# Optimization experiments

Measured on AMD Instinct MI355X. Metric: run time of the kernel, lower is better.

## Reference

```python
import jax, jax.numpy as jnp
import numpy as np
import math

D, H = 128, 8
B, LC, LQ = 8, 512, 64


def pos_signal(channels, length):
    # tensor2tensor timing signal, returned as [C, L]
    pos = jnp.arange(length, dtype=jnp.float32)
    nts = channels // 2
    inc = math.log(1.0e4) / (nts - 1)
    inv = jnp.exp(jnp.arange(nts, dtype=jnp.float32) * -inc)
    st = pos[:, None] * inv[None, :]                      # [L, nts]
    sig = jnp.concatenate([jnp.sin(st), jnp.cos(st)], 1)  # [L, C]
    return sig.T


def mask_logits(t, m):
    return t * m + (1.0 - m) * -1e30


def ln_c(x, g, b):  # LayerNorm over channel dim of [B, D, L]
    mu = jnp.mean(x, axis=1, keepdims=True)
    var = jnp.mean((x - mu) ** 2, axis=1, keepdims=True)
    return (x - mu) / jnp.sqrt(var + 1e-5) * g[None, :, None] + b[None, :, None]


def conv1x1(x, w, b=None):  # x [B, I, L], w [O, I]
    y = jnp.einsum('oi,bil->bol', w, x)
    return y if b is None else y + b[None, :, None]


def dw_sep_conv(x, dw, pw, pwb):  # depthwise (k, no bias) -> pointwise (bias) -> relu
    k = dw.shape[-1]
    y = jax.lax.conv_general_dilated(x, dw[:, None, :], (1,), [(k // 2, k // 2)],
        dimension_numbers=('NCH', 'OIH', 'NCH'), feature_group_count=x.shape[1])
    return jax.nn.relu(conv1x1(y, pw, pwb))


def self_attention(x, mem_w, q_w, mask, n_head):  # x [B, D, L]
    b, d, L = x.shape
    dh = d // n_head
    mem = jnp.einsum('oi,bil->blo', mem_w, x)  # [B, L, 2D]
    q = jnp.einsum('oi,bil->blo', q_w, x)      # [B, L, D]
    def heads(t):
        return t.reshape(b, L, n_head, dh).transpose(0, 2, 1, 3)  # [B, H, L, dh]
    Qh = heads(q) * dh ** -0.5
    K = heads(mem[..., :d])
    V = heads(mem[..., d:])
    logits = jnp.einsum('bhqe,bhke->bhqk', Qh, K)
    logits = mask_logits(logits, mask[:, None, None, :])
    w = jax.nn.softmax(logits, axis=-1)
    o = jnp.einsum('bhqk,bhke->bhqe', w, V)
    return o.transpose(0, 2, 1, 3).reshape(b, L, d).transpose(0, 2, 1)


def encoder_block(x, mask, p, n_head):
    out = x + pos_signal(x.shape[1], x.shape[2])[None]
    n_conv = p['dw'].shape[0]
    for i in range(n_conv):
        res = out
        out = ln_c(out, p['lnc_g'][i], p['lnc_b'][i])
        out = dw_sep_conv(out, p['dw'][i], p['pw'][i], p['pw_b'][i]) + res
    res = out
    out = ln_c(out, p['ln1_g'], p['ln1_b'])
    out = self_attention(out, p['mem_w'], p['q_w'], mask, n_head) + res
    res = out
    out = ln_c(out, p['ln2_g'], p['ln2_b'])
    out = jax.nn.relu(conv1x1(out, p['ffn1_w'], p['ffn1_b']))
    out = conv1x1(out, p['ffn2_w'], p['ffn2_b'])
    return out + res


def cq_attention(Ce, Qe, cmask, qmask, w4C, w4Q, w4mlu, cq_b):
    Cx = Ce.transpose(0, 2, 1)   # [B, Lc, 2D]
    Qx = Qe.transpose(0, 2, 1)   # [B, Lq, 2D]
    s0 = jnp.einsum('bld,d->bl', Cx, w4C)[:, :, None]
    s1 = jnp.einsum('bqd,d->bq', Qx, w4Q)[:, None, :]
    s2 = jnp.einsum('bld,bqd->blq', Cx * w4mlu[None, None, :], Qx)
    S = s0 + s1 + s2 + cq_b
    S1 = jax.nn.softmax(mask_logits(S, qmask[:, None, :]), axis=2)
    S2 = jax.nn.softmax(mask_logits(S, cmask[:, :, None]), axis=1)
    A = jnp.einsum('blq,bqd->bld', S1, Qx)
    Bt = jnp.einsum('blq,bmq,bmd->bld', S1, S2, Cx)  # (S1 @ S2^T) @ C
    out = jnp.concatenate([Cx, A, Cx * A, Cx * Bt], axis=2)
    return out.transpose(0, 2, 1)  # [B, 8D, Lc]


def _forward(C, Q, maskC, maskQ, e_dw, e_pw, e_pw_b, e_lnc_g, e_lnc_b, e_mem_w, e_q_w,
             e_ffn1_w, e_ffn1_b, e_ffn2_w, e_ffn2_b, e_ln1_g, e_ln1_b, e_ln2_g, e_ln2_b,
             w4C, w4Q, w4mlu, cq_b, resizer_w,
             m_dw, m_pw, m_pw_b, m_lnc_g, m_lnc_b, m_mem_w, m_q_w,
             m_ffn1_w, m_ffn1_b, m_ffn2_w, m_ffn2_b, m_ln1_g, m_ln1_b, m_ln2_g, m_ln2_b):
    ep = dict(dw=e_dw, pw=e_pw, pw_b=e_pw_b, lnc_g=e_lnc_g, lnc_b=e_lnc_b,
              mem_w=e_mem_w, q_w=e_q_w, ffn1_w=e_ffn1_w, ffn1_b=e_ffn1_b,
              ffn2_w=e_ffn2_w, ffn2_b=e_ffn2_b, ln1_g=e_ln1_g, ln1_b=e_ln1_b,
              ln2_g=e_ln2_g, ln2_b=e_ln2_b)
    mp = dict(dw=m_dw, pw=m_pw, pw_b=m_pw_b, lnc_g=m_lnc_g, lnc_b=m_lnc_b,
              mem_w=m_mem_w, q_w=m_q_w, ffn1_w=m_ffn1_w, ffn1_b=m_ffn1_b,
              ffn2_w=m_ffn2_w, ffn2_b=m_ffn2_b, ln1_g=m_ln1_g, ln1_b=m_ln1_b,
              ln2_g=m_ln2_g, ln2_b=m_ln2_b)
    Ce = encoder_block(C, maskC, ep, H)
    Qe = encoder_block(Q, maskQ, ep, H)
    Ce = jnp.concatenate([Ce, C], axis=1)  # encode_fusion -> [B, 2D, Lc]
    Qe = jnp.concatenate([Qe, Q], axis=1)
    X = cq_attention(Ce, Qe, maskC, maskQ, w4C, w4Q, w4mlu, cq_b)
    X = jnp.concatenate([X, Ce], axis=1)   # match_fusion -> [B, 10D, Lc]
    M0 = conv1x1(X, resizer_w)             # [B, D, Lc]

    def run(m):
        def step(carry, p):
            return encoder_block(carry, maskC, p, H), None
        m, _ = jax.lax.scan(step, m, mp)
        return m

    M1 = run(M0)
    M2 = run(M1)
    M3 = run(M2)
    return M1, M2, M3


def setup_inputs() -> dict:
    key = jax.random.key(0)
    ks = iter(jax.random.split(key, 48))
    def rn(shape, scale):
        return jax.random.normal(next(ks), shape, dtype=jnp.float32) * scale
    s1 = 1.0 / math.sqrt(D)
    s2 = 1.0 / math.sqrt(2 * D)
    f32 = jnp.float32
    return dict(
        C=rn((B, D, LC), 1.0), Q=rn((B, D, LQ), 1.0),
        maskC=jnp.ones((B, LC), f32), maskQ=jnp.ones((B, LQ), f32),
        e_dw=rn((4, D, 7), 1.0 / math.sqrt(7)), e_pw=rn((4, D, D), s1),
        e_pw_b=jnp.zeros((4, D), f32), e_lnc_g=jnp.ones((4, D), f32), e_lnc_b=jnp.zeros((4, D), f32),
        e_mem_w=rn((2 * D, D), s1), e_q_w=rn((D, D), s1),
        e_ffn1_w=rn((D, D), s1), e_ffn1_b=jnp.zeros((D,), f32),
        e_ffn2_w=rn((D, D), s1), e_ffn2_b=jnp.zeros((D,), f32),
        e_ln1_g=jnp.ones((D,), f32), e_ln1_b=jnp.zeros((D,), f32),
        e_ln2_g=jnp.ones((D,), f32), e_ln2_b=jnp.zeros((D,), f32),
        w4C=rn((2 * D,), s2), w4Q=rn((2 * D,), s2), w4mlu=rn((2 * D,), s2),
        cq_b=jnp.zeros((1,), f32),
        resizer_w=rn((D, 10 * D), 1.0 / math.sqrt(10 * D)),
        m_dw=rn((7, 2, D, 5), 1.0 / math.sqrt(5)), m_pw=rn((7, 2, D, D), s1),
        m_pw_b=jnp.zeros((7, 2, D), f32), m_lnc_g=jnp.ones((7, 2, D), f32), m_lnc_b=jnp.zeros((7, 2, D), f32),
        m_mem_w=rn((7, 2 * D, D), s1), m_q_w=rn((7, D, D), s1),
        m_ffn1_w=rn((7, D, D), s1), m_ffn1_b=jnp.zeros((7, D), f32),
        m_ffn2_w=rn((7, D, D), s1), m_ffn2_b=jnp.zeros((7, D), f32),
        m_ln1_g=jnp.ones((7, D), f32), m_ln1_b=jnp.zeros((7, D), f32),
        m_ln2_g=jnp.ones((7, D), f32), m_ln2_b=jnp.zeros((7, D), f32),
    )


def reference(C, Q, maskC, maskQ, e_dw, e_pw, e_pw_b, e_lnc_g, e_lnc_b, e_mem_w, e_q_w,
              e_ffn1_w, e_ffn1_b, e_ffn2_w, e_ffn2_b, e_ln1_g, e_ln1_b, e_ln2_g, e_ln2_b,
              w4C, w4Q, w4mlu, cq_b, resizer_w,
              m_dw, m_pw, m_pw_b, m_lnc_g, m_lnc_b, m_mem_w, m_q_w,
              m_ffn1_w, m_ffn1_b, m_ffn2_w, m_ffn2_b, m_ln1_g, m_ln1_b, m_ln2_g, m_ln2_b):
    return _forward(C, Q, maskC, maskQ, e_dw, e_pw, e_pw_b, e_lnc_g, e_lnc_b, e_mem_w, e_q_w,
                    e_ffn1_w, e_ffn1_b, e_ffn2_w, e_ffn2_b, e_ln1_g, e_ln1_b, e_ln2_g, e_ln2_b,
                    w4C, w4Q, w4mlu, cq_b, resizer_w,
                    m_dw, m_pw, m_pw_b, m_lnc_g, m_lnc_b, m_mem_w, m_q_w,
                    m_ffn1_w, m_ffn1_b, m_ffn2_w, m_ffn2_b, m_ln1_g, m_ln1_b, m_ln2_g, m_ln2_b)
```

## Files before the change

### kernel.cpp

```cpp
#include <hip/hip_runtime.h>
#include <math.h>

#define D_  128
#define B_  8
#define H_  8
#define LC_ 512
#define LQ_ 64

typedef float f32x4 __attribute__((ext_vector_type(4)));
typedef short bf16x8 __attribute__((ext_vector_type(8)));
typedef short short4v __attribute__((ext_vector_type(4)));
typedef unsigned short ushortT;

__device__ inline short bfr(float x) {
  unsigned u = __float_as_uint(x);
  u += 0x7fff + ((u >> 16) & 1);
  return (short)(u >> 16);
}
__device__ inline float bfi(ushortT u) {
  return __uint_as_float(((unsigned)u) << 16);
}

__device__ inline bf16x8 mk8(short4v lo, short4v hi) {
  bf16x8 r;
// ... 6 lines not shown
  short4v lo = *(const short4v*)(row + koff);
  short4v hi = *(const short4v*)(row + koff + 16);
  return mk8(lo, hi);
}
__device__ inline bf16x8 ldB2(const ushortT* plo, const ushortT* phi) {
  short4v lo = *(const short4v*)plo;
  short4v hi = *(const short4v*)phi;
  return mk8(lo, hi);
}

__global__ void k_prep(const float* a0, const float* a1, const float* a2,
                       const float* a3, const float* a4, const float* a5,
                       const float* a6, const float* a7, const float* a8,
                       const float* a9, const float* a10, ushortT* dst) {
  int i = blockIdx.x * 256 + threadIdx.x;
  if (i >= 1114112) return;
  const float* s; int lo;
  if      (i <   65536) { s = a0;  lo = i; }
  else if (i <   98304) { s = a1;  lo = i - 65536; }
  else if (i <  114688) { s = a2;  lo = i - 98304; }
  else if (i <  131072) { s = a3;  lo = i - 114688; }
  else if (i <  147456) { s = a4;  lo = i - 131072; }
  else if (i <  311296) { s = a5;  lo = i - 147456; }
  else if (i <  540672) { s = a6;  lo = i - 311296; }
  else if (i <  770048) { s = a7;  lo = i - 540672; }
  else if (i <  884736) { s = a8;  lo = i - 770048; }
  else if (i <  999424) { s = a9;  lo = i - 884736; }
  else                  { s = a10; lo = i - 999424; }
  dst[i] = (ushortT)bfr(s[lo]);
}

template <int KK, int ADDPOS>
__global__ __launch_bounds__(256) void k_fusedconv(
    const float* __restrict__ x, float* __restrict__ yout,
    const float* __restrict__ dw1, const ushortT* __restrict__ pw1,
    const float* __restrict__ pb1, const float* __restrict__ g1,
    const float* __restrict__ be1,
    const float* __restrict__ dw2, const ushortT* __restrict__ pw2,
    const float* __restrict__ pb2, const float* __restrict__ g2w,
    const float* __restrict__ be2, int L) {
  const int HALO = KK / 2;
  const int W1 = 32 + 2 * HALO;
  __shared__ __align__(16) float raw[128 * 40];
  __shared__ __align__(16) ushortT l1o[128 * 36];
  __shared__ __align__(16) ushortT xbf1[32 * 32 * 4];
  __shared__ float mu1[40], rs1[40], mu2[32], rs2[32], ps[160], psq[160];
  ushortT* xbf2 = (ushortT*)raw;
  int l0 = blockIdx.x * 16;
  int o0 = blockIdx.y * 64;
  int b = blockIdx.z;
  int tid = threadIdx.x;
  for (int idx = tid; idx < 128 * W1; idx += 256) {
    int d = idx / W1, c = idx - d * W1;
    int gl = l0 - 8 - HALO + c;
    float v = 0.f;
    if (gl >= 0 && gl < L) {
      v = x[((size_t)b * 128 + d) * L + gl];
      if (ADDPOS) {
        int j = d & 63;
        float arg = (float)gl * expf(-(float)j * 0.14619588f);
        v += (d < 64) ? sinf(arg) : cosf(arg);
      }
    }
    raw[d * 40 + c] = v;
  }
  __syncthreads();
  if (tid < 4 * W1) {
    int c = tid % W1, hh = tid / W1;
    float s = 0.f, s2 = 0.f;
    for (int d = hh * 32; d < hh * 32 + 32; d++) {
      float v = raw[d * 40 + c];
      s += v; s2 += v * v;
    }
    ps[tid] = s; psq[tid] = s2;
  }
  __syncthreads();
  if (tid < W1) {
    float s = ps[tid] + ps[tid + W1] + ps[tid + 2 * W1] + ps[tid + 3 * W1];
    float s2 = psq[tid] + psq[tid + W1] + psq[tid + 2 * W1] + psq[tid + 3 * W1];
    float mu = s * (1.f / 128.f);
    float var = fmaxf(s2 * (1.f / 128.f) - mu * mu, 0.f);
// ... 98 lines not shown
          int gl = l0 + cc2 + t - HALO;
          float lv = 0.f;
          if (gl >= 0 && gl < L)
            lv = (bfi(l1o[d * 36 + c1]) - mu2[c1]) * rs2[c1] * gg + bb;
          acc += wr[t] * lv;
        }
        pk[e] = bfr(acc);
      }
      *(short4v*)&xbf2[(((db2 * 2 + kq) * 16) + cc2) * 4] = pk;
    }
  }
  __syncthreads();
  {
    f32x4 a2 = {0.f, 0.f, 0.f, 0.f};
    const ushortT* arow = pw2 + (size_t)(o0 + 16 * w + r) * 128;
#pragma unroll
    for (int kk = 0; kk < 4; kk++) {
      bf16x8 a = ldA(arow, kk * 32 + g2 * 4);
      bf16x8 bb = ldB2(&xbf2[(((kk * 8 + g2) * 16) + r) * 4],
                       &xbf2[(((kk * 8 + 4 + g2) * 16) + r) * 4]);
      a2 = __builtin_amdgcn_mfma_f32_16x16x32_bf16(a, bb, a2, 0, 0, 0);
    }
#pragma unroll
    for (int p = 0; p < 4; p++) {
      int o = o0 + 16 * w + g2 * 4 + p;
      yout[((size_t)b * 128 + o) * L + l0 + r] =
          fmaxf(a2[p] + pb2[o], 0.f) + bfi(l1o[o * 36 + 8 + r]);
    }
  }
}

template <int KK, int ADDPOS>
__global__ __launch_bounds__(1024) void k_convproj1024(
    const float* __restrict__ x, float* __restrict__ yout,
    const float* __restrict__ dw1, const ushortT* __restrict__ pw1,
    const float* __restrict__ pb1, const float* __restrict__ g1,
    const float* __restrict__ be1,
    const float* __restrict__ dw2, const ushortT* __restrict__ pw2,
    const float* __restrict__ pb2, const float* __restrict__ g2w,
    const float* __restrict__ be2,
    const ushortT* __restrict__ memw, const ushortT* __restrict__ qw,
    const float* __restrict__ g3, const float* __restrict__ be3,
    float* __restrict__ mkv, float* __restrict__ qp, int L) {
  const int HALO = KK / 2;
  const int W1 = 32 + 2 * HALO;
  __shared__ __align__(16) float raw[128 * 40];
  __shared__ __align__(16) ushortT l1o[128 * 36];
  __shared__ __align__(16) ushortT xbf1[32 * 32 * 4];
  __shared__ __align__(16) ushortT c2o[128 * 16];
  __shared__ float mu1[40], rs1[40], mu2[32], rs2[32], mu3[16], rs3[16];
  __shared__ float ps[160], psq[160];
  ushortT* xbf2 = (ushortT*)raw;
  ushortT* xbf3 = (ushortT*)(raw + 4096);
  int l0 = blockIdx.x * 16;
  int b = blockIdx.z;
  int tid = threadIdx.x;
  for (int idx = tid; idx < 128 * W1; idx += 1024) {
    int d = idx / W1, c = idx - d * W1;
    int gl = l0 - 8 - HALO + c;
    float v = 0.f;
    if (gl >= 0 && gl < L) {
      v = x[((size_t)b * 128 + d) * L + gl];
      if (ADDPOS) {
        int j = d & 63;
        float arg = (float)gl * expf(-(float)j * 0.14619588f);
        v += (d < 64) ? sinf(arg) : cosf(arg);
      }
    }
    raw[d * 40 + c] = v;
  }
  __syncthreads();
  if (tid < 4 * W1) {
    int c = tid % W1, hh = tid / W1;
    float s = 0.f, s2 = 0.f;
    for (int d = hh * 32; d < hh * 32 + 32; d++) {
      float v = raw[d * 40 + c];
      s += v; s2 += v * v;
    }
    ps[tid] = s; psq[tid] = s2;
  }
  __syncthreads();
  if (tid < W1) {
    float s = ps[tid] + ps[tid + W1] + ps[tid + 2 * W1] + ps[tid + 3 * W1];
    float s2 = psq[tid] + psq[tid + W1] + psq[tid + 2 * W1] + psq[tid + 3 * W1];
    float mu = s * (1.f / 128.f);
    float var = fmaxf(s2 * (1.f / 128.f) - mu * mu, 0.f);
    mu1[tid] = mu; rs1[tid] = rsqrtf(var + 1e-5f);
// ... 122 lines not shown
    float var = fmaxf(s2 * (1.f / 128.f) - mu * mu, 0.f);
    mu3[tid] = mu; rs3[tid] = rsqrtf(var + 1e-5f);
  }
  __syncthreads();
  for (int idx = tid; idx < 2048; idx += 1024) {
    int d = idx >> 4, c = idx & 15;
    float val = (bfi(c2o[d * 16 + c]) - mu3[c]) * rs3[c] * g3[d] + be3[d];
    xbf3[(((d >> 2) * 16) + c) * 4 + (d & 3)] = (ushortT)bfr(val);
  }
  __syncthreads();
#pragma unroll
  for (int t = 0; t < 2; t++) {
    int mt = w + 16 * t;
    if (mt < 24) {
      const ushortT* arow; float* outp; int obase, O;
      if (mt < 16) { arow = memw + (size_t)(mt * 16 + r) * 128; outp = mkv; obase = mt * 16; O = 256; }
      else         { arow = qw + (size_t)((mt - 16) * 16 + r) * 128; outp = qp; obase = (mt - 16) * 16; O = 128; }
      f32x4 acc = {0.f, 0.f, 0.f, 0.f};
#pragma unroll
      for (int kk = 0; kk < 4; kk++) {
        bf16x8 a = ldA(arow, kk * 32 + g2 * 4);
        bf16x8 bb = ldB2(&xbf3[(((kk * 8 + g2) * 16) + r) * 4],
                         &xbf3[(((kk * 8 + 4 + g2) * 16) + r) * 4]);
        acc = __builtin_amdgcn_mfma_f32_16x16x32_bf16(a, bb, acc, 0, 0, 0);
      }
#pragma unroll
      for (int p = 0; p < 4; p++)
        outp[((size_t)b * O + obase + g2 * 4 + p) * L + l0 + r] = acc[p];
    }
  }
}

template <int NCH, int WOUT>
__global__ __launch_bounds__(1024) void k_attnffn(
    const float* __restrict__ memKV, const float* __restrict__ qp,
    const float* __restrict__ mask, float* __restrict__ cur,
    const ushortT* __restrict__ w1bf, const float* __restrict__ b1,
    const ushortT* __restrict__ w2bf, const float* __restrict__ b2,
    const float* __restrict__ g, const float* __restrict__ be,
    float* __restrict__ wout, int L) {
  __shared__ float msh[8][64], ssh[8][64], Osh[8][64][4];
  __shared__ float updT[128 * 16];
  __shared__ __align__(16) ushortT xbf[32 * 16 * 4];
  __shared__ __align__(16) ushortT midbf[32 * 16 * 4];
  __shared__ float mu_s[16], rs_s[16], ps[1024], psq[1024];
  int q0 = blockIdx.x * 16;
  int b = blockIdx.z;
  int tid = threadIdx.x;
  int w = tid >> 6;
  int h = w & 7, kh = w >> 3;
  int lane = tid & 63;
  int g2 = lane >> 4, r = lane & 15;
  const float* qb = qp + ((size_t)b * 128 + h * 16) * L;
  const float* kb = memKV + ((size_t)b * 256 + h * 16) * L;
  const float* vb = memKV + ((size_t)b * 256 + 128 + h * 16) * L;
  const float* mk = mask + (size_t)b * L;
  int qcol = q0 + r;
  bf16x8 qf;
#pragma unroll
  for (int j = 0; j < 4; j++)
    qf[j] = bfr(qb[(size_t)(g2 * 4 + j) * L + qcol] * 0.25f);
  qf[4] = 0; qf[5] = 0; qf[6] = 0; qf[7] = 0;
  float m_run = -INFINITY, ssum = 0.f;
  f32x4 O = {0.f, 0.f, 0.f, 0.f};
  int kbeg = kh * (L / 2), kend = (kh + 1) * (L / 2);
  for (int k0 = kbeg; k0 < kend; k0 += NCH * 16) {
    f32x4 sd[NCH];
#pragma unroll
    for (int mc = 0; mc < NCH; mc++) {
      bf16x8 kf;
      int krow = k0 + mc * 16 + r;
#pragma unroll
      for (int j = 0; j < 4; j++)
        kf[j] = bfr(kb[(size_t)(g2 * 4 + j) * L + krow]);
      kf[4] = 0; kf[5] = 0; kf[6] = 0; kf[7] = 0;
      f32x4 z = {0.f, 0.f, 0.f, 0.f};
      sd[mc] = __builtin_amdgcn_mfma_f32_16x16x32_bf16(kf, qf, z, 0, 0, 0);
    }
    float tm = -INFINITY;
#pragma unroll
    for (int mc = 0; mc < NCH; mc++) {
// ... 10 lines not shown
    float nm = fmaxf(m_run, tm);
    float c = __expf(m_run - nm);
    ssum *= c;
    O[0] *= c; O[1] *= c; O[2] *= c; O[3] *= c;
    float psum = 0.f;
    bf16x8 pf[NCH / 2];
#pragma unroll
    for (int c2 = 0; c2 < NCH / 2; c2++) {
#pragma unroll
      for (int j = 0; j < 4; j++) {
        float e0 = __expf(sd[2 * c2][j] - nm);
        float e1 = __expf(sd[2 * c2 + 1][j] - nm);
        psum += e0 + e1;
        pf[c2][j] = bfr(e0);
        pf[c2][j + 4] = bfr(e1);
      }
    }
    psum += __shfl_xor(psum, 16);
    psum += __shfl_xor(psum, 32);
    ssum += psum;
#pragma unroll
    for (int c2 = 0; c2 < NCH / 2; c2++) {
      const float* vrow = vb + (size_t)r * L + k0 + c2 * 32 + g2 * 4;
      float4 v0 = *(const float4*)vrow;
      float4 v1 = *(const float4*)(vrow + 16);
      bf16x8 vf;
      vf[0] = bfr(v0.x); vf[1] = bfr(v0.y); vf[2] = bfr(v0.z); vf[3] = bfr(v0.w);
      vf[4] = bfr(v1.x); vf[5] = bfr(v1.y); vf[6] = bfr(v1.z); vf[7] = bfr(v1.w);
      O = __builtin_amdgcn_mfma_f32_16x16x32_bf16(vf, pf[c2], O, 0, 0, 0);
    }
    m_run = nm;
  }
  if (kh == 1) {
    msh[h][lane] = m_run;
    ssh[h][lane] = ssum;
#pragma unroll
    for (int p = 0; p < 4; p++) Osh[h][lane][p] = O[p];
  }
  __syncthreads();
  if (kh == 0) {
    float mB = msh[h][lane], sB = ssh[h][lane];
    float nm = fmaxf(m_run, mB);
    float cA = __expf(m_run - nm), cB = __expf(mB - nm);
    float inv = 1.f / (ssum * cA + sB * cB);
#pragma unroll
    for (int p = 0; p < 4; p++) {
      int d = h * 16 + g2 * 4 + p;
      float ov = (O[p] * cA + Osh[h][lane][p] * cB) * inv;
      updT[d * 16 + r] = cur[((size_t)b * 128 + d) * L + qcol] + ov;
    }
  }
  __syncthreads();
  {
    int c = tid & 15, hh = tid >> 4;
    float s = 0.f, s2 = 0.f;
    for (int d = hh * 2; d < hh * 2 + 2; d++) {
      float v = updT[d * 16 + c];
      s += v; s2 += v * v;
    }
    ps[tid] = s; psq[tid] = s2;
  }
  __syncthreads();
  if (tid < 16) {
    float s = 0.f, s2 = 0.f;
    for (int hh = 0; hh < 64; hh++) { s += ps[hh * 16 + tid]; s2 += psq[hh * 16 + tid]; }
    float mu = s * (1.f / 128.f);
    float var = fmaxf(s2 * (1.f / 128.f) - mu * mu, 0.f);
    mu_s[tid] = mu; rs_s[tid] = rsqrtf(var + 1e-5f);
  }
  __syncthreads();
  for (int idx = tid; idx < 2048; idx += 1024) {
    int d = idx >> 4, c = idx & 15;
    float val = (updT[d * 16 + c] - mu_s[c]) * rs_s[c] * g[d] + be[d];
    xbf[(((d >> 2) * 16) + c) * 4 + (d & 3)] = (ushortT)bfr(val);
  }
  __syncthreads();
  if (w < 8) {
    f32x4 acc = {0.f, 0.f, 0.f, 0.f};
    const ushortT* ar = w1bf + (size_t)(16 * w + r) * 128;
#pragma unroll
    for (int kk = 0; kk < 4; kk++) {
// ... 1 lines not shown
      bf16x8 bb = ldB2(&xbf[(((kk * 8 + g2) * 16) + r) * 4],
                       &xbf[(((kk * 8 + 4 + g2) * 16) + r) * 4]);
      acc = __builtin_amdgcn_mfma_f32_16x16x32_bf16(a, bb, acc, 0, 0, 0);
    }
#pragma unroll
    for (int p = 0; p < 4; p++) {
      int dmid = 16 * w + g2 * 4 + p;
      float val = fmaxf(acc[p] + b1[dmid], 0.f);
      midbf[(((4 * w + g2) * 16) + r) * 4 + p] = (ushortT)bfr(val);
    }
  }
  __syncthreads();
  if (w < 8) {
    f32x4 a2 = {0.f, 0.f, 0.f, 0.f};
    const ushortT* ar = w2bf + (size_t)(16 * w + r) * 128;
#pragma unroll
    for (int kk = 0; kk < 4; kk++) {
      bf16x8 a = ldA(ar, kk * 32 + g2 * 4);
      bf16x8 bb = ldB2(&midbf[(((kk * 8 + g2) * 16) + r) * 4],
                       &midbf[(((kk * 8 + 4 + g2) * 16) + r) * 4]);
      a2 = __builtin_amdgcn_mfma_f32_16x16x32_bf16(a, bb, a2, 0, 0, 0);
    }
#pragma unroll
    for (int p = 0; p < 4; p++) {
      int o = 16 * w + g2 * 4 + p;
      size_t pos = ((size_t)b * 128 + o) * L + q0 + r;
      float val = a2[p] + b2[o] + updT[o * 16 + r];
      cur[pos] = val;
      if (WOUT) wout[pos] = val;
    }
  }
}


__global__ void k_concat2(const float* __restrict__ x1, const float* __restrict__ x2,
                          float* __restrict__ out, int L, int total) {
  int idx = blockIdx.x * 256 + threadIdx.x;
  if (idx >= total) return;
  int l = idx % L;
  int c = (idx / L) & 255;
  int b = idx / (L * 256);
  float v = (c < 128) ? x1[((size_t)b * 128 + c) * L + l]
                      : x2[((size_t)b * 128 + (c - 128)) * L + l];
  out[idx] = v;
}

__global__ void k_cqSrow(const float* __restrict__ Ce, const float* __restrict__ Qe,
                         const float* __restrict__ w4C, const float* __restrict__ w4Q,
                         const float* __restrict__ w4mlu, const float* __restrict__ cqb,
                         const float* __restrict__ qmask,
                         float* __restrict__ S, float* __restrict__ S1) {
  int idx = blockIdx.x * 256 + threadIdx.x;
  int q = idx & 63;
  int l = (idx >> 6) % LC_;
  int b = (idx >> 6) / LC_;
  const float* ce = Ce + (size_t)b * 256 * LC_ + l;
  const float* qe = Qe + (size_t)b * 256 * LQ_ + q;
  float acc = 0.f, a0 = 0.f, a1 = 0.f;
#pragma unroll 8
  for (int j = 0; j < 256; j++) {
    float cv = ce[(size_t)j * LC_];
    float qv = qe[(size_t)j * LQ_];
    acc += cv * w4mlu[j] * qv;
    a0 += cv * w4C[j];
    a1 += qv * w4Q[j];
  }
  float sv = acc + a0 + a1 + cqb[0];
  S[idx] = sv;
  float mv = qmask[b * LQ_ + q];
  float v = sv * mv + (1.f - mv) * (-1e30f);
  float mx = v;
  for (int off = 32; off; off >>= 1) mx = fmaxf(mx, __shfl_xor(mx, off));
  float p = expf(v - mx);
  float s = p;
  for (int off = 32; off; off >>= 1) s += __shfl_xor(s, off);
  S1[idx] = p / s;
}
// ... 40 lines not shown
  float acc = 0.f;
#pragma unroll 8
  for (int l = 0; l < LC_; l++) acc += s2[(size_t)l * LQ_] * ce[l];
  Y[idx] = acc;
}

__global__ __launch_bounds__(256) void k_cqAB(
    const float* __restrict__ S1, const float* __restrict__ Qe, const float* __restrict__ Y,
    float* __restrict__ A, float* __restrict__ Bt) {
  __shared__ float s1s[64][65];
  int l0 = blockIdx.x * 64;
  int b = blockIdx.z;
  int tid = threadIdx.x;
  for (int idx = tid; idx < 64 * 64; idx += 256) {
    int l = idx >> 6, q = idx & 63;
    s1s[l][q] = S1[((size_t)b * LC_ + l0 + l) * LQ_ + q];
  }
  __syncthreads();
  int ll = tid & 63, jj = tid >> 6;
  int j = blockIdx.y * 4 + jj;
  const float* qe = Qe + ((size_t)b * 256 + j) * LQ_;
  const float* yb = Y + ((size_t)b * 256 + j) * LQ_;
  float a = 0.f, bt = 0.f;
#pragma unroll 8
  for (int q = 0; q < 64; q++) {
    float sv = s1s[ll][q];
    a += sv * qe[q];
    bt += sv * yb[q];
  }
  A[((size_t)b * 256 + j) * LC_ + l0 + ll] = a;
  Bt[((size_t)b * 256 + j) * LC_ + l0 + ll] = bt;
}

__global__ __launch_bounds__(256) void k_resizer_mfma(
    const float* __restrict__ Ce, const float* __restrict__ A,
    const float* __restrict__ Bt, const ushortT* __restrict__ wbf,
    float* __restrict__ y) {
  __shared__ __align__(16) ushortT xbf[16 * 16 * 4];
  int l0 = blockIdx.x * 16;
  int o0 = blockIdx.y * 64;
  int b = blockIdx.z;
  int tid = threadIdx.x;
  int w = tid >> 6, lane = tid & 63, g2 = lane >> 4, r = lane & 15;
  const ushortT* arow = wbf + (size_t)(o0 + 16 * w + r) * 1280;
  f32x4 acc0 = {0.f, 0.f, 0.f, 0.f};
  for (int kt = 0; kt < 1280; kt += 64) {
    __syncthreads();
    for (int idx = tid; idx < 1024; idx += 256) {
      int kloc = idx >> 4, cc = idx & 15;
      int ch = kt + kloc;
      int seg = ch >> 8;
      int j = ch & 255;
      size_t p = ((size_t)b * 256 + j) * LC_ + l0 + cc;
      float v;
      if (seg == 0 || seg == 4) v = Ce[p];
      else if (seg == 1) v = A[p];
      else if (seg == 2) v = Ce[p] * A[p];
      else v = Ce[p] * Bt[p];
      xbf[(((kloc >> 2) * 16) + cc) * 4 + (kloc & 3)] = (ushortT)bfr(v);
    }
    __syncthreads();
#pragma unroll
    for (int kk2 = 0; kk2 < 2; kk2++) {
      bf16x8 a = ldA(arow, kt + kk2 * 32 + g2 * 4);
      bf16x8 b0 = ldB2(&xbf[(((kk2 * 8 + g2) * 16) + r) * 4],
                       &xbf[(((kk2 * 8 + 4 + g2) * 16) + r) * 4]);
      acc0 = __builtin_amdgcn_mfma_f32_16x16x32_bf16(a, b0, acc0, 0, 0, 0);
    }
  }
#pragma unroll
  for (int p = 0; p < 4; p++) {
    int o = o0 + 16 * w + g2 * 4 + p;
    y[((size_t)b * D_ + o) * LC_ + l0 + r] = acc0[p];
  }
}


struct BlkP {
  int k;
  const float* lnc_g[4]; const float* lnc_b[4];
  const float* dw[4]; const ushortT* pw[4]; const float* pw_b[4];
  const ushortT* mem_w; const ushortT* q_w;
  const float* ln1_g; const float* ln1_b;
  const ushortT* ffn1_w; const float* ffn1_b;
  const ushortT* ffn2_w; const float* ffn2_b;
  const float* ln2_g; const float* ln2_b;
};

static void conv_pair_only(hipStream_t st, const float* in, float* out, int L,
                           const BlkP& P, int i0, bool addpos) {
  dim3 gc(L / 16, 2, B_);
  if (addpos)
    k_fusedconv<7, 1><<<gc, 256, 0, st>>>(in, out,
        P.dw[i0], P.pw[i0], P.pw_b[i0], P.lnc_g[i0], P.lnc_b[i0],
        P.dw[i0+1], P.pw[i0+1], P.pw_b[i0+1], P.lnc_g[i0+1], P.lnc_b[i0+1], L);
  else
    k_fusedconv<7, 0><<<gc, 256, 0, st>>>(in, out,
        P.dw[i0], P.pw[i0], P.pw_b[i0], P.lnc_g[i0], P.lnc_b[i0],
        P.dw[i0+1], P.pw[i0+1], P.pw_b[i0+1], P.lnc_g[i0+1], P.lnc_b[i0+1], L);
}

template <int KK, int ADDPOS>
static void convproj(hipStream_t st, const float* in, float* out, float* mkv,
                     float* qpb, int L, const BlkP& P, int i0) {
  k_convproj1024<KK, ADDPOS><<<dim3(L / 16, 1, B_), 1024, 0, st>>>(in, out,
      P.dw[i0], P.pw[i0], P.pw_b[i0], P.lnc_g[i0], P.lnc_b[i0],
      P.dw[i0+1], P.pw[i0+1], P.pw_b[i0+1], P.lnc_g[i0+1], P.lnc_b[i0+1],
      P.mem_w, P.q_w, P.ln1_g, P.ln1_b, mkv, qpb, L);
}

static void attnffn(hipStream_t st, float* cur, float* mkv, float* qpb,
                    const float* mask, int L, const BlkP& P, float* wout) {
  dim3 g(L / 16, 1, B_);
  if (L == LC_) {
    if (wout)
      k_attnffn<8, 1><<<g, 1024, 0, st>>>(mkv, qpb, mask, cur,
          P.ffn1_w, P.ffn1_b, P.ffn2_w, P.ffn2_b, P.ln2_g, P.ln2_b, wout, L);
    else
      k_attnffn<8, 0><<<g, 1024, 0, st>>>(mkv, qpb, mask, cur,
          P.ffn1_w, P.ffn1_b, P.ffn2_w, P.ffn2_b, P.ln2_g, P.ln2_b, nullptr, L);
  } else {
    k_attnffn<2, 0><<<g, 1024, 0, st>>>(mkv, qpb, mask, cur,
        P.ffn1_w, P.ffn1_b, P.ffn2_w, P.ffn2_b, P.ln2_g, P.ln2_b, nullptr, L);
  }
}

extern "C" void kernel_launch(void* const* d_in, const int* in_sizes, int n_in,
                              void* d_out, int out_size, void* d_ws, size_t ws_size,
                              hipStream_t stream) {
  (void)in_sizes; (void)n_in; (void)out_size; (void)ws_size;
  const float* C        = (const float*)d_in[0];
  const float* Q        = (const float*)d_in[1];
  const float* maskC    = (const float*)d_in[2];
  const float* maskQ    = (const float*)d_in[3];
  const float* e_dw     = (const float*)d_in[4];
  const float* e_pw     = (const float*)d_in[5];
  const float* e_pw_b   = (const float*)d_in[6];
  const float* e_lnc_g  = (const float*)d_in[7];
  const float* e_lnc_b  = (const float*)d_in[8];
  const float* e_mem_w  = (const float*)d_in[9];
  const float* e_q_w    = (const float*)d_in[10];
  const float* e_ffn1_w = (const float*)d_in[11];
  const float* e_ffn1_b = (const float*)d_in[12];
  const float* e_ffn2_w = (const float*)d_in[13];
  const float* e_ffn2_b = (const float*)d_in[14];
  const float* e_ln1_g  = (const float*)d_in[15];
  const float* e_ln1_b  = (const float*)d_in[16];
  const float* e_ln2_g  = (const float*)d_in[17];
  const float* e_ln2_b  = (const float*)d_in[18];
  const float* w4C      = (const float*)d_in[19];
  const float* w4Q      = (const float*)d_in[20];
  const float* w4mlu    = (const float*)d_in[21];
  const float* cq_b     = (const float*)d_in[22];
  const float* resizer_w= (const float*)d_in[23];
  const float* m_dw     = (const float*)d_in[24];
  const float* m_pw     = (const float*)d_in[25];
  const float* m_pw_b   = (const float*)d_in[26];
  const float* m_lnc_g  = (const float*)d_in[27];
// ... 6 lines not shown
  const float* m_ffn2_b = (const float*)d_in[34];
  const float* m_ln1_g  = (const float*)d_in[35];
  const float* m_ln1_b  = (const float*)d_in[36];
  const float* m_ln2_g  = (const float*)d_in[37];
  const float* m_ln2_b  = (const float*)d_in[38];

  float* ws = (float*)d_ws;
  const size_t SB = (size_t)B_ * D_ * LC_;
  float* cur  = ws;
  float* aux  = cur + SB;
  float* mkv  = aux + SB;
  float* qpb  = mkv + 2 * SB;
  float* Ce   = qpb + SB;
  float* Qe   = Ce + 2 * SB;
  float* Sbuf = Qe + (size_t)B_ * 256 * LQ_;
  float* S1   = Sbuf + (size_t)B_ * LC_ * LQ_;
  float* S2   = S1 + (size_t)B_ * LC_ * LQ_;
  float* Yb   = S2 + (size_t)B_ * LC_ * LQ_;
  float* Mb   = Yb + (size_t)B_ * 256 * LQ_;
  float* Ab   = mkv;
  float* Bb   = cur;
  ushortT* wb = (ushortT*)(Mb + SB);
  ushortT* w_epw  = wb;
  ushortT* w_emem = wb + 65536;
  ushortT* w_eq   = wb + 98304;
  ushortT* w_ef1  = wb + 114688;
  ushortT* w_ef2  = wb + 131072;
  ushortT* w_rsz  = wb + 147456;
  ushortT* w_mpw  = wb + 311296;
  ushortT* w_mmem = wb + 540672;
  ushortT* w_mq   = wb + 770048;
  ushortT* w_mf1  = wb + 884736;
  ushortT* w_mf2  = wb + 999424;

  k_prep<<<(1114112 + 255) / 256, 256, 0, stream>>>(
      e_pw, e_mem_w, e_q_w, e_ffn1_w, e_ffn2_w, resizer_w,
      m_pw, m_mem_w, m_q_w, m_ffn1_w, m_ffn2_w, wb);

  BlkP ep{};
  ep.k = 7;
  for (int i = 0; i < 4; i++) {
    ep.lnc_g[i] = e_lnc_g + i * 128;
    ep.lnc_b[i] = e_lnc_b + i * 128;
    ep.dw[i]    = e_dw + i * 128 * 7;
    ep.pw[i]    = w_epw + (size_t)i * 128 * 128;
    ep.pw_b[i]  = e_pw_b + i * 128;
  }
  ep.mem_w = w_emem; ep.q_w = w_eq;
  ep.ln1_g = e_ln1_g; ep.ln1_b = e_ln1_b;
  ep.ffn1_w = w_ef1; ep.ffn1_b = e_ffn1_b;
  ep.ffn2_w = w_ef2; ep.ffn2_b = e_ffn2_b;
  ep.ln2_g = e_ln2_g; ep.ln2_b = e_ln2_b;

  conv_pair_only(stream, C, cur, LC_, ep, 0, true);
  convproj<7, 0>(stream, cur, aux, mkv, qpb, LC_, ep, 2);
  attnffn(stream, aux, mkv, qpb, maskC, LC_, ep, nullptr);
  {
    int tot = B_ * 256 * LC_;
    k_concat2<<<(tot + 255) / 256, 256, 0, stream>>>(aux, C, Ce, LC_, tot);
  }
  conv_pair_only(stream, Q, cur, LQ_, ep, 0, true);
  convproj<7, 0>(stream, cur, aux, mkv, qpb, LQ_, ep, 2);
  attnffn(stream, aux, mkv, qpb, maskQ, LQ_, ep, nullptr);
  {
    int tot = B_ * 256 * LQ_;
    k_concat2<<<(tot + 255) / 256, 256, 0, stream>>>(aux, Q, Qe, LQ_, tot);
  }

  k_cqSrow<<<(B_ * LC_ * LQ_) / 256, 256, 0, stream>>>(Ce, Qe, w4C, w4Q, w4mlu, cq_b, maskQ, Sbuf, S1);
  k_softmax_col<<<B_ * LQ_, 256, 0, stream>>>(Sbuf, maskC, S2);
  k_cqY<<<(B_ * 256 * LQ_) / 256, 256, 0, stream>>>(S2, Ce, Yb);
  k_cqAB<<<dim3(LC_ / 64, 64, B_), 256, 0, stream>>>(S1, Qe, Yb, Ab, Bb);
  k_resizer_mfma<<<dim3(LC_ / 16, 2, B_), 256, 0, stream>>>(Ce, Ab, Bb, w_rsz, Mb);

  float* out = (float*)d_out;
  float* bufs[2] = {cur, aux};
  int cb = 0;
  const float* src = Mb;
  for (int r = 0; r < 3; r++) {
    for (int bi = 0; bi < 7; bi++) {
      BlkP mp{};
      mp.k = 5;
      for (int ci = 0; ci < 2; ci++) {
        int pc = bi * 2 + ci;
        mp.lnc_g[ci] = m_lnc_g + pc * 128;
        mp.lnc_b[ci] = m_lnc_b + pc * 128;
        mp.dw[ci]    = m_dw + pc * 128 * 5;
        mp.pw[ci]    = w_mpw + (size_t)pc * 128 * 128;
        mp.pw_b[ci]  = m_pw_b + pc * 128;
      }
      mp.mem_w  = w_mmem + (size_t)bi * 256 * 128;
      mp.q_w    = w_mq + (size_t)bi * 128 * 128;
      mp.ffn1_w = w_mf1 + (size_t)bi * 128 * 128;
      mp.ffn1_b = m_ffn1_b + bi * 128;
      mp.ffn2_w = w_mf2 + (size_t)bi * 128 * 128;
      mp.ffn2_b = m_ffn2_b + bi * 128;
      mp.ln1_g = m_ln1_g + bi * 128; mp.ln1_b = m_ln1_b + bi * 128;
      mp.ln2_g = m_ln2_g + bi * 128; mp.ln2_b = m_ln2_b + bi * 128;
      float* ob = bufs[cb];
      convproj<5, 1>(stream, src, ob, mkv, qpb, LC_, mp, 0);
      float* wout = (bi == 6) ? out + (size_t)r * SB : nullptr;
      attnffn(stream, ob, mkv, qpb, maskC, LC_, mp, wout);
      src = ob;
      cb ^= 1;
    }
  }
}
```

Measured before the change: 1.395 ms.

## Batch context and query encoder kernels into shared launches; widen resizer block

The embedding-encoder conv, convproj, attention-FFN and concat kernels now take both the context and query tensors and dispatch on block index. This merges the separate C and Q launches into one each, with separate Q scratch buffers. The attention kernel body becomes a device function over raw shared memory so the two sequence lengths can share one kernel. The resizer now uses 512-thread blocks covering all 128 outputs with a larger K tile. The goal is fewer launches and better GPU fill for the small query pass, at the cost of branchy kernels and extra workspace.

Measured after the change: 1.335 ms. 4.4% less time.

```diff
diff --git a/kernel.cpp b/kernel.cpp
--- a/kernel.cpp
+++ b/kernel.cpp
@@ -62,13 +62,14 @@
 
 template <int KK, int ADDPOS>
 __global__ __launch_bounds__(256) void k_fusedconv(
-    const float* __restrict__ x, float* __restrict__ yout,
+    const float* __restrict__ xC, float* __restrict__ yC,
+    const float* __restrict__ xQ, float* __restrict__ yQ,
     const float* __restrict__ dw1, const ushortT* __restrict__ pw1,
     const float* __restrict__ pb1, const float* __restrict__ g1,
     const float* __restrict__ be1,
     const float* __restrict__ dw2, const ushortT* __restrict__ pw2,
     const float* __restrict__ pb2, const float* __restrict__ g2w,
-    const float* __restrict__ be2, int L) {
+    const float* __restrict__ be2, int ntC) {
   const int HALO = KK / 2;
   const int W1 = 32 + 2 * HALO;
   __shared__ __align__(16) float raw[128 * 40];
@@ -76,7 +77,10 @@
   __shared__ __align__(16) ushortT xbf1[32 * 32 * 4];
   __shared__ float mu1[40], rs1[40], mu2[32], rs2[32], ps[160], psq[160];
   ushortT* xbf2 = (ushortT*)raw;
-  int l0 = blockIdx.x * 16;
+  int bx = blockIdx.x;
+  const float* x; float* yout; int l0, L;
+  if (bx < ntC) { x = xC; yout = yC; l0 = bx * 16; L = LC_; }
+  else          { x = xQ; yout = yQ; l0 = (bx - ntC) * 16; L = LQ_; }
   int o0 = blockIdx.y * 64;
   int b = blockIdx.z;
   int tid = threadIdx.x;
@@ -241,7 +245,10 @@
 
 template <int KK, int ADDPOS>
 __global__ __launch_bounds__(1024) void k_convproj1024(
-    const float* __restrict__ x, float* __restrict__ yout,
+    const float* __restrict__ xC, float* __restrict__ yC,
+    float* __restrict__ mkvC, float* __restrict__ qpC,
+    const float* __restrict__ xQ, float* __restrict__ yQ,
+    float* __restrict__ mkvQ, float* __restrict__ qpQ,
     const float* __restrict__ dw1, const ushortT* __restrict__ pw1,
     const float* __restrict__ pb1, const float* __restrict__ g1,
     const float* __restrict__ be1,
@@ -249,8 +256,7 @@
     const float* __restrict__ pb2, const float* __restrict__ g2w,
     const float* __restrict__ be2,
     const ushortT* __restrict__ memw, const ushortT* __restrict__ qw,
-    const float* __restrict__ g3, const float* __restrict__ be3,
-    float* __restrict__ mkv, float* __restrict__ qp, int L) {
+    const float* __restrict__ g3, const float* __restrict__ be3, int ntC) {
   const int HALO = KK / 2;
   const int W1 = 32 + 2 * HALO;
   __shared__ __align__(16) float raw[128 * 40];
@@ -261,7 +267,10 @@
   __shared__ float ps[160], psq[160];
   ushortT* xbf2 = (ushortT*)raw;
   ushortT* xbf3 = (ushortT*)(raw + 4096);
-  int l0 = blockIdx.x * 16;
+  int bx = blockIdx.x;
+  const float* x; float* yout; float* mkv; float* qp; int l0, L;
+  if (bx < ntC) { x = xC; yout = yC; mkv = mkvC; qp = qpC; l0 = bx * 16; L = LC_; }
+  else          { x = xQ; yout = yQ; mkv = mkvQ; qp = qpQ; l0 = (bx - ntC) * 16; L = LQ_; }
   int b = blockIdx.z;
   int tid = threadIdx.x;
   for (int idx = tid; idx < 128 * W1; idx += 1024) {
@@ -450,21 +459,21 @@
 }
 
 template <int NCH, int WOUT>
-__global__ __launch_bounds__(1024) void k_attnffn(
-    const float* __restrict__ memKV, const float* __restrict__ qp,
-    const float* __restrict__ mask, float* __restrict__ cur,
-    const ushortT* __restrict__ w1bf, const float* __restrict__ b1,
-    const ushortT* __restrict__ w2bf, const float* __restrict__ b2,
-    const float* __restrict__ g, const float* __restrict__ be,
-    float* __restrict__ wout, int L) {
-  __shared__ float msh[8][64], ssh[8][64], Osh[8][64][4];
-  __shared__ float updT[128 * 16];
-  __shared__ __align__(16) ushortT xbf[32 * 16 * 4];
-  __shared__ __align__(16) ushortT midbf[32 * 16 * 4];
-  __shared__ float mu_s[16], rs_s[16], ps[1024], psq[1024];
-  int q0 = blockIdx.x * 16;
-  int b = blockIdx.z;
-  int tid = threadIdx.x;
+__device__ __forceinline__ void attn_body(
+    char* smem, const float* memKV, const float* qp, const float* mask,
+    float* cur, const ushortT* w1bf, const float* b1,
+    const ushortT* w2bf, const float* b2,
+    const float* g, const float* be, float* wout, int q0, int b, int L, int tid) {
+  float* msh = (float*)smem;
+  float* ssh = (float*)(smem + 2048);
+  float* OshF = (float*)(smem + 4096);
+  float* updT = (float*)(smem + 12288);
+  ushortT* xbf = (ushortT*)(smem + 20480);
+  ushortT* midbf = (ushortT*)(smem + 24576);
+  float* mu_s = (float*)(smem + 28672);
+  float* rs_s = (float*)(smem + 28736);
+  float* ps = (float*)(smem + 28800);
+  float* psq = (float*)(smem + 32896);
   int w = tid >> 6;
   int h = w & 7, kh = w >> 3;
   int lane = tid & 63;
@@ -541,21 +550,21 @@
     m_run = nm;
   }
   if (kh == 1) {
-    msh[h][lane] = m_run;
-    ssh[h][lane] = ssum;
-#pragma unroll
-    for (int p = 0; p < 4; p++) Osh[h][lane][p] = O[p];
+    msh[h * 64 + lane] = m_run;
+    ssh[h * 64 + lane] = ssum;
+#pragma unroll
+    for (int p = 0; p < 4; p++) OshF[(h * 64 + lane) * 4 + p] = O[p];
   }
   __syncthreads();
   if (kh == 0) {
-    float mB = msh[h][lane], sB = ssh[h][lane];
+    float mB = msh[h * 64 + lane], sB = ssh[h * 64 + lane];
     float nm = fmaxf(m_run, mB);
     float cA = __expf(m_run - nm), cB = __expf(mB - nm);
     float inv = 1.f / (ssum * cA + sB * cB);
 #pragma unroll
     for (int p = 0; p < 4; p++) {
       int d = h * 16 + g2 * 4 + p;
-      float ov = (O[p] * cA + Osh[h][lane][p] * cB) * inv;
+      float ov = (O[p] * cA + OshF[(h * 64 + lane) * 4 + p] * cB) * inv;
       updT[d * 16 + r] = cur[((size_t)b * 128 + d) * L + qcol] + ov;
     }
   }
@@ -623,17 +632,57 @@
   }
 }
 
-
-__global__ void k_concat2(const float* __restrict__ x1, const float* __restrict__ x2,
-                          float* __restrict__ out, int L, int total) {
+template <int WOUT>
+__global__ __launch_bounds__(1024) void k_attnffn_m(
+    const float* memKV, const float* qp, const float* mask, float* cur,
+    const ushortT* w1bf, const float* b1, const ushortT* w2bf, const float* b2,
+    const float* g, const float* be, float* wout) {
+  __shared__ __align__(16) char smem[36992];
+  attn_body<8, WOUT>(smem, memKV, qp, mask, cur, w1bf, b1, w2bf, b2, g, be,
+                     wout, blockIdx.x * 16, blockIdx.z, LC_, threadIdx.x);
+}
+
+__global__ __launch_bounds__(1024) void k_attnffn_in(
+    const float* mkvC, const float* qpC, const float* maskC, float* curC,
+    const float* mkvQ, const float* qpQ, const float* maskQ, float* curQ,
+    const ushortT* w1bf, const float* b1, const ushortT* w2bf, const float* b2,
+    const float* g, const float* be, int ntC) {
+  __shared__ __align__(16) char smem[36992];
+  int bx = blockIdx.x;
+  if (bx < ntC)
+    attn_body<8, 0>(smem, mkvC, qpC, maskC, curC, w1bf, b1, w2bf, b2, g, be,
+                    nullptr, bx * 16, blockIdx.z, LC_, threadIdx.x);
+  else
+    attn_body<2, 0>(smem, mkvQ, qpQ, maskQ, curQ, w1bf, b1, w2bf, b2, g, be,
+                    nullptr, (bx - ntC) * 16, blockIdx.z, LQ_, threadIdx.x);
+}
+
+
+__global__ void k_concat2m(const float* __restrict__ x1C, const float* __restrict__ x2C,
+                           float* __restrict__ outC,
+                           const float* __restrict__ x1Q, const float* __restrict__ x2Q,
+                           float* __restrict__ outQ) {
   int idx = blockIdx.x * 256 + threadIdx.x;
-  if (idx >= total) return;
-  int l = idx % L;
-  int c = (idx / L) & 255;
-  int b = idx / (L * 256);
-  float v = (c < 128) ? x1[((size_t)b * 128 + c) * L + l]
-                      : x2[((size_t)b * 128 + (c - 128)) * L + l];
-  out[idx] = v;
+  const int tot1 = B_ * 256 * LC_;
+  const int tot2 = B_ * 256 * LQ_;
+  if (idx < tot1) {
+    int l = idx % LC_;
+    int c = (idx / LC_) & 255;
+    int b = idx / (LC_ * 256);
+    float v = (c < 128) ? x1C[((size_t)b * 128 + c) * LC_ + l]
+                        : x2C[((size_t)b * 128 + (c - 128)) * LC_ + l];
+    outC[idx] = v;
+  } else {
+    int i2 = idx - tot1;
+    if (i2 < tot2) {
+      int l = i2 % LQ_;
+      int c = (i2 / LQ_) & 255;
+      int b = i2 / (LQ_ * 256);
+      float v = (c < 128) ? x1Q[((size_t)b * 128 + c) * LQ_ + l]
+                          : x2Q[((size_t)b * 128 + (c - 128)) * LQ_ + l];
+      outQ[i2] = v;
+    }
+  }
 }
 
 __global__ void k_cqSrow(const float* __restrict__ Ce, const float* __restrict__ Qe,
@@ -740,23 +789,22 @@
   Bt[((size_t)b * 256 + j) * LC_ + l0 + ll] = bt;
 }
 
-__global__ __launch_bounds__(256) void k_resizer_mfma(
+__global__ __launch_bounds__(512) void k_resizer512(
     const float* __restrict__ Ce, const float* __restrict__ A,
     const float* __restrict__ Bt, const ushortT* __restrict__ wbf,
     float* __restrict__ y) {
-  __shared__ __align__(16) ushortT xbf[16 * 16 * 4];
+  __shared__ __align__(16) ushortT xbf[32 * 16 * 4];
   int l0 = blockIdx.x * 16;
-  int o0 = blockIdx.y * 64;
   int b = blockIdx.z;
   int tid = threadIdx.x;
   int w = tid >> 6, lane = tid & 63, g2 = lane >> 4, r = lane & 15;
-  const ushortT* arow = wbf + (size_t)(o0 + 16 * w + r) * 1280;
-  f32x4 acc0 = {0.f, 0.f, 0.f, 0.f};
-  for (int kt = 0; kt < 1280; kt += 64) {
+  const ushortT* arow = wbf + (size_t)(16 * w + r) * 1280;
+  f32x4 acc = {0.f, 0.f, 0.f, 0.f};
+  for (int kt = 0; kt < 1280; kt += 128) {
     __syncthreads();
-    for (int idx = tid; idx < 1024; idx += 256) {
-      int kloc = idx >> 4, cc = idx & 15;
-      int ch = kt + kloc;
+    for (int idx = tid; idx < 2048; idx += 512) {
+      int kl = idx >> 4, cc = idx & 15;
+      int ch = kt + kl;
       int seg = ch >> 8;
       int j = ch & 255;
       size_t p = ((size_t)b * 256 + j) * LC_ + l0 + cc;
@@ -765,73 +813,24 @@
       else if (seg == 1) v = A[p];
       else if (seg == 2) v = Ce[p] * A[p];
       else v = Ce[p] * Bt[p];
-      xbf[(((kloc >> 2) * 16) + cc) * 4 + (kloc & 3)] = (ushortT)bfr(v);
+      xbf[((kl >> 2) * 16 + cc) * 4 + (kl & 3)] = (ushortT)bfr(v);
     }
     __syncthreads();
 #pragma unroll
-    for (int kk2 = 0; kk2 < 2; kk2++) {
+    for (int kk2 = 0; kk2 < 4; kk2++) {
       bf16x8 a = ldA(arow, kt + kk2 * 32 + g2 * 4);
       bf16x8 b0 = ldB2(&xbf[(((kk2 * 8 + g2) * 16) + r) * 4],
                        &xbf[(((kk2 * 8 + 4 + g2) * 16) + r) * 4]);
-      acc0 = __builtin_amdgcn_mfma_f32_16x16x32_bf16(a, b0, acc0, 0, 0, 0);
+      acc = __builtin_amdgcn_mfma_f32_16x16x32_bf16(a, b0, acc, 0, 0, 0);
     }
   }
 #pragma unroll
   for (int p = 0; p < 4; p++) {
-    int o = o0 + 16 * w + g2 * 4 + p;
-    y[((size_t)b * D_ + o) * LC_ + l0 + r] = acc0[p];
-  }
-}
-
-
-struct BlkP {
-  int k;
-  const float* lnc_g[4]; const float* lnc_b[4];
-  const float* dw[4]; const ushortT* pw[4]; const float* pw_b[4];
-  const ushortT* mem_w; const ushortT* q_w;
-  const float* ln1_g; const float* ln1_b;
-  const ushortT* ffn1_w; const float* ffn1_b;
-  const ushortT* ffn2_w; const float* ffn2_b;
-  const float* ln2_g; const float* ln2_b;
-};
-
-static void conv_pair_only(hipStream_t st, const float* in, float* out, int L,
-                           const BlkP& P, int i0, bool addpos) {
-  dim3 gc(L / 16, 2, B_);
-  if (addpos)
-    k_fusedconv<7, 1><<<gc, 256, 0, st>>>(in, out,
-        P.dw[i0], P.pw[i0], P.pw_b[i0], P.lnc_g[i0], P.lnc_b[i0],
-        P.dw[i0+1], P.pw[i0+1], P.pw_b[i0+1], P.lnc_g[i0+1], P.lnc_b[i0+1], L);
-  else
-    k_fusedconv<7, 0><<<gc, 256, 0, st>>>(in, out,
-        P.dw[i0], P.pw[i0], P.pw_b[i0], P.lnc_g[i0], P.lnc_b[i0],
-        P.dw[i0+1], P.pw[i0+1], P.pw_b[i0+1], P.lnc_g[i0+1], P.lnc_b[i0+1], L);
-}
-
-template <int KK, int ADDPOS>
-static void convproj(hipStream_t st, const float* in, float* out, float* mkv,
-                     float* qpb, int L, const BlkP& P, int i0) {
-  k_convproj1024<KK, ADDPOS><<<dim3(L / 16, 1, B_), 1024, 0, st>>>(in, out,
-      P.dw[i0], P.pw[i0], P.pw_b[i0], P.lnc_g[i0], P.lnc_b[i0],
-      P.dw[i0+1], P.pw[i0+1], P.pw_b[i0+1], P.lnc_g[i0+1], P.lnc_b[i0+1],
-      P.mem_w, P.q_w, P.ln1_g, P.ln1_b, mkv, qpb, L);
-}
-
-static void attnffn(hipStream_t st, float* cur, float* mkv, float* qpb,
-                    const float* mask, int L, const BlkP& P, float* wout) {
-  dim3 g(L / 16, 1, B_);
-  if (L == LC_) {
-    if (wout)
-      k_attnffn<8, 1><<<g, 1024, 0, st>>>(mkv, qpb, mask, cur,
-          P.ffn1_w, P.ffn1_b, P.ffn2_w, P.ffn2_b, P.ln2_g, P.ln2_b, wout, L);
-    else
-      k_attnffn<8, 0><<<g, 1024, 0, st>>>(mkv, qpb, mask, cur,
-          P.ffn1_w, P.ffn1_b, P.ffn2_w, P.ffn2_b, P.ln2_g, P.ln2_b, nullptr, L);
-  } else {
-    k_attnffn<2, 0><<<g, 1024, 0, st>>>(mkv, qpb, mask, cur,
-        P.ffn1_w, P.ffn1_b, P.ffn2_w, P.ffn2_b, P.ln2_g, P.ln2_b, nullptr, L);
-  }
-}
+    int o = 16 * w + g2 * 4 + p;
+    y[((size_t)b * D_ + o) * LC_ + l0 + r] = acc[p];
+  }
+}
+
 
 extern "C" void kernel_launch(void* const* d_in, const int* in_sizes, int n_in,
                               void* d_out, int out_size, void* d_ws, size_t ws_size,
@@ -904,46 +903,36 @@
   ushortT* w_mq   = wb + 770048;
   ushortT* w_mf1  = wb + 884736;
   ushortT* w_mf2  = wb + 999424;
+  float* after_wb = (float*)(wb + 1114112);
+  float* curQ  = after_wb;
+  float* auxQ  = curQ + 65536;
+  float* mkvQ  = auxQ + 65536;
+  float* qpbQ  = mkvQ + 131072;
 
   k_prep<<<(1114112 + 255) / 256, 256, 0, stream>>>(
       e_pw, e_mem_w, e_q_w, e_ffn1_w, e_ffn2_w, resizer_w,
       m_pw, m_mem_w, m_q_w, m_ffn1_w, m_ffn2_w, wb);
 
-  BlkP ep{};
-  ep.k = 7;
-  for (int i = 0; i < 4; i++) {
-    ep.lnc_g[i] = e_lnc_g + i * 128;
-    ep.lnc_b[i] = e_lnc_b + i * 128;
-    ep.dw[i]    = e_dw + i * 128 * 7;
-    ep.pw[i]    = w_epw + (size_t)i * 128 * 128;
-    ep.pw_b[i]  = e_pw_b + i * 128;
-  }
-  ep.mem_w = w_emem; ep.q_w = w_eq;
-  ep.ln1_g = e_ln1_g; ep.ln1_b = e_ln1_b;
-  ep.ffn1_w = w_ef1; ep.ffn1_b = e_ffn1_b;
-  ep.ffn2_w = w_ef2; ep.ffn2_b = e_ffn2_b;
-  ep.ln2_g = e_ln2_g; ep.ln2_b = e_ln2_b;
-
-  conv_pair_only(stream, C, cur, LC_, ep, 0, true);
-  convproj<7, 0>(stream, cur, aux, mkv, qpb, LC_, ep, 2);
-  attnffn(stream, aux, mkv, qpb, maskC, LC_, ep, nullptr);
-  {
-    int tot = B_ * 256 * LC_;
-    k_concat2<<<(tot + 255) / 256, 256, 0, stream>>>(aux, C, Ce, LC_, tot);
-  }
-  conv_pair_only(stream, Q, cur, LQ_, ep, 0, true);
-  convproj<7, 0>(stream, cur, aux, mkv, qpb, LQ_, ep, 2);
-  attnffn(stream, aux, mkv, qpb, maskQ, LQ_, ep, nullptr);
-  {
-    int tot = B_ * 256 * LQ_;
-    k_concat2<<<(tot + 255) / 256, 256, 0, stream>>>(aux, Q, Qe, LQ_, tot);
-  }
+  k_fusedconv<7, 1><<<dim3(36, 2, B_), 256, 0, stream>>>(
+      C, cur, Q, curQ,
+      e_dw + 0 * 896, w_epw + 0, e_pw_b + 0, e_lnc_g + 0, e_lnc_b + 0,
+      e_dw + 1 * 896, w_epw + 16384, e_pw_b + 128, e_lnc_g + 128, e_lnc_b + 128, 32);
+  k_convproj1024<7, 0><<<dim3(36, 1, B_), 1024, 0, stream>>>(
+      cur, aux, mkv, qpb, curQ, auxQ, mkvQ, qpbQ,
+      e_dw + 2 * 896, w_epw + 32768, e_pw_b + 256, e_lnc_g + 256, e_lnc_b + 256,
+      e_dw + 3 * 896, w_epw + 49152, e_pw_b + 384, e_lnc_g + 384, e_lnc_b + 384,
+      w_emem, w_eq, e_ln1_g, e_ln1_b, 32);
+  k_attnffn_in<<<dim3(36, 1, B_), 1024, 0, stream>>>(
+      mkv, qpb, maskC, aux, mkvQ, qpbQ, maskQ, auxQ,
+      w_ef1, e_ffn1_b, w_ef2, e_ffn2_b, e_ln2_g, e_ln2_b, 32);
+  k_concat2m<<<(B_ * 256 * (LC_ + LQ_) + 255) / 256, 256, 0, stream>>>(
+      aux, C, Ce, auxQ, Q, Qe);
 
   k_cqSrow<<<(B_ * LC_ * LQ_) / 256, 256, 0, stream>>>(Ce, Qe, w4C, w4Q, w4mlu, cq_b, maskQ, Sbuf, S1);
   k_softmax_col<<<B_ * LQ_, 256, 0, stream>>>(Sbuf, maskC, S2);
   k_cqY<<<(B_ * 256 * LQ_) / 256, 256, 0, stream>>>(S2, Ce, Yb);
   k_cqAB<<<dim3(LC_ / 64, 64, B_), 256, 0, stream>>>(S1, Qe, Yb, Ab, Bb);
-  k_resizer_mfma<<<dim3(LC_ / 16, 2, B_), 256, 0, stream>>>(Ce, Ab, Bb, w_rsz, Mb);
+  k_resizer512<<<dim3(LC_ / 16, 1, B_), 512, 0, stream>>>(Ce, Ab, Bb, w_rsz, Mb);
 
   float* out = (float*)d_out;
   float* bufs[2] = {cur, aux};
@@ -951,28 +940,28 @@
   const float* src = Mb;
   for (int r = 0; r < 3; r++) {
     for (int bi = 0; bi < 7; bi++) {
-      BlkP mp{};
-      mp.k = 5;
-      for (int ci = 0; ci < 2; ci++) {
-        int pc = bi * 2 + ci;
-        mp.lnc_g[ci] = m_lnc_g + pc * 128;
-        mp.lnc_b[ci] = m_lnc_b + pc * 128;
-        mp.dw[ci]    = m_dw + pc * 128 * 5;
-        mp.pw[ci]    = w_mpw + (size_t)pc * 128 * 128;
-        mp.pw_b[ci]  = m_pw_b + pc * 128;
-      }
-      mp.mem_w  = w_mmem + (size_t)bi * 256 * 128;
-      mp.q_w    = w_mq + (size_t)bi * 128 * 128;
-      mp.ffn1_w = w_mf1 + (size_t)bi * 128 * 128;
-      mp.ffn1_b = m_ffn1_b + bi * 128;
-      mp.ffn2_w = w_mf2 + (size_t)bi * 128 * 128;
-      mp.ffn2_b = m_ffn2_b + bi * 128;
-      mp.ln1_g = m_ln1_g + bi * 128; mp.ln1_b = m_ln1_b + bi * 128;
-      mp.ln2_g = m_ln2_g + bi * 128; mp.ln2_b = m_ln2_b + bi * 128;
+      int pc0 = bi * 2, pc1 = bi * 2 + 1;
       float* ob = bufs[cb];
-      convproj<5, 1>(stream, src, ob, mkv, qpb, LC_, mp, 0);
-      float* wout = (bi == 6) ? out + (size_t)r * SB : nullptr;
-      attnffn(stream, ob, mkv, qpb, maskC, LC_, mp, wout);
+      k_convproj1024<5, 1><<<dim3(32, 1, B_), 1024, 0, stream>>>(
+          src, ob, mkv, qpb, src, ob, mkv, qpb,
+          m_dw + (size_t)pc0 * 640, w_mpw + (size_t)pc0 * 16384, m_pw_b + pc0 * 128,
+          m_lnc_g + pc0 * 128, m_lnc_b + pc0 * 128,
+          m_dw + (size_t)pc1 * 640, w_mpw + (size_t)pc1 * 16384, m_pw_b + pc1 * 128,
+          m_lnc_g + pc1 * 128, m_lnc_b + pc1 * 128,
+          w_mmem + (size_t)bi * 32768, w_mq + (size_t)bi * 16384,
+          m_ln1_g + bi * 128, m_ln1_b + bi * 128, 32);
+      if (bi == 6)
+        k_attnffn_m<1><<<dim3(32, 1, B_), 1024, 0, stream>>>(
+            mkv, qpb, maskC, ob,
+            w_mf1 + (size_t)bi * 16384, m_ffn1_b + bi * 128,
+            w_mf2 + (size_t)bi * 16384, m_ffn2_b + bi * 128,
+            m_ln2_g + bi * 128, m_ln2_b + bi * 128, out + (size_t)r * SB);
+      else
+        k_attnffn_m<0><<<dim3(32, 1, B_), 1024, 0, stream>>>(
+            mkv, qpb, maskC, ob,
+            w_mf1 + (size_t)bi * 16384, m_ffn1_b + bi * 128,
+            w_mf2 + (size_t)bi * 16384, m_ffn2_b + bi * 128,
+            m_ln2_g + bi * 128, m_ln2_b + bi * 128, nullptr);
       src = ob;
       cb ^= 1;
     }
```
